# Optimization experiments

Hardware: AMD Instinct MI355X
Metric: run time of the kernel (lower is better)

## Reference

```python
import jax, jax.numpy as jnp
import numpy as np

T = 35        # points per voxel
D, H, W = 10, 400, 352  # voxel grid (KITTI car setting)
EPS = 1e-5    # BatchNorm eps


def setup_inputs() -> dict:
    key = jax.random.key(0)
    ks = jax.random.split(key, 10)
    K = 15000  # non-empty voxels in the frame
    feature = jax.random.normal(ks[0], (K, T, 7), jnp.float32)
    # realistic padding: each voxel has 5..35 valid points, rest zero
    npts = jax.random.randint(ks[1], (K,), 5, T + 1)
    valid = jnp.arange(T)[None, :] < npts[:, None]
    feature = feature * valid[:, :, None].astype(jnp.float32)
    c_b = jnp.zeros((K, 1), jnp.int32)
    c_d = jax.random.randint(ks[2], (K, 1), 0, D).astype(jnp.int32)
    c_h = jax.random.randint(ks[3], (K, 1), 0, H).astype(jnp.int32)
    c_w = jax.random.randint(ks[4], (K, 1), 0, W).astype(jnp.int32)
    coordinate = jnp.concatenate([c_b, c_d, c_h, c_w], axis=1)
    W1 = jax.random.normal(ks[5], (7, 16), jnp.float32) * 0.1
    b1 = jnp.zeros((16,), jnp.float32)
    g1 = jnp.ones((16,), jnp.float32)
    be1 = jnp.zeros((16,), jnp.float32)
    W2 = jax.random.normal(ks[6], (32, 64), jnp.float32) * 0.1
    b2 = jnp.zeros((64,), jnp.float32)
    g2 = jnp.ones((64,), jnp.float32)
    be2 = jnp.zeros((64,), jnp.float32)
    return {"feature": feature, "coordinate": coordinate, "bs": 1,
            "W1": W1, "b1": b1, "g1": g1, "be1": be1,
            "W2": W2, "b2": b2, "g2": g2, "be2": be2}


def _vfe(x, mask, Wm, b, g, be):
    # Linear + ReLU per point: [K, T, cin] -> [K, T, cmid]
    pw = jax.nn.relu(jnp.einsum('ktc,cd->ktd', x, Wm) + b)
    # BatchNorm1d (training mode): per-channel stats over (K, T), biased var
    mu = pw.mean(axis=(0, 1))
    var = pw.var(axis=(0, 1))
    pw = (pw - mu) * jax.lax.rsqrt(var + EPS) * g + be
    # max over points, broadcast-concat (VoxelNet VFE)
    agg = pw.max(axis=1, keepdims=True)               # [K, 1, cmid]
    cat = jnp.concatenate([pw, jnp.broadcast_to(agg, pw.shape)], axis=-1)
    return cat * mask  # mask padded points


def reference(feature, coordinate, bs, W1, b1, g1, be1, W2, b2, g2, be2):
    # mask: point is valid if its channel-wise max != 0 (as in original)
    vmax = feature.max(axis=2, keepdims=True)          # [K, T, 1]
    mask = (vmax != 0).astype(feature.dtype)
    x = _vfe(feature, mask, W1, b1, g1, be1)           # [K, T, 32]
    x = _vfe(x, mask, W2, b2, g2, be2)                 # [K, T, 128]
    voxelwise = x.max(axis=1)                          # [K, 128]
    # scatter into dense grid (sparse COO -> to_dense sums duplicates)
    out = jnp.zeros((bs, D, H, W, 128), feature.dtype)
    out = out.at[coordinate[:, 0], coordinate[:, 1],
                 coordinate[:, 2], coordinate[:, 3]].add(voxelwise)
    return out
```

## Files before the change

### kernel.cpp

```cpp
#include <hip/hip_runtime.h>
#include <math.h>

#define KVOX 15000
#define TP 35
#define CIN 7
#define CM1 16
#define CM2 64
#define NPTS (KVOX * TP)
#define DD 10
#define HH 400
#define WWID 352
#define NCELL (DD * HH * WWID)
#define EPSBN 1e-5f
#define NB1 256
#define NBV 3750
#define NBW 2048

typedef float vfloat4 __attribute__((ext_vector_type(4)));
typedef int   vint4   __attribute__((ext_vector_type(4)));
typedef short bf16x8  __attribute__((ext_vector_type(8)));
typedef float f32x4   __attribute__((ext_vector_type(4)));

__device__ inline unsigned short f2b(float x)
{
    unsigned int u = __float_as_uint(x);
    unsigned int r = (u + 0x7FFFu + ((u >> 16) & 1u)) >> 16;
    return (unsigned short)r;
}

#define NT4 (NCELL / 4)
__global__ __launch_bounds__(256) void init_kernel(vint4* __restrict__ table4)
{
    int i = blockIdx.x * 256 + threadIdx.x;
    table4[i] = (vint4){0x7FFFFFFF, 0x7FFFFFFF, 0x7FFFFFFF, 0x7FFFFFFF};
}

__global__ __launch_bounds__(256) void stats1_kernel(
    const float* __restrict__ feat, const int* __restrict__ coord,
    const float* __restrict__ W1, const float* __restrict__ b1,
    float* __restrict__ partial1, int* __restrict__ table)
{
    __shared__ float w1s[CIN * CM1];
    __shared__ float b1s[CM1];
    __shared__ float red[4][32];
    int tid = threadIdx.x;
    if (tid < CIN * CM1) w1s[tid] = W1[tid];
    if (tid < CM1) b1s[tid] = b1[tid];

    int g = blockIdx.x * 256 + tid;
    if (g < KVOX) {
        int cell = (coord[g * 4 + 1] * HH + coord[g * 4 + 2]) * WWID + coord[g * 4 + 3];
        atomicMin(&table[cell], g);
    }
    __syncthreads();

    float s[CM1], q[CM1];
#pragma unroll
    for (int c = 0; c < CM1; ++c) { s[c] = 0.f; q[c] = 0.f; }

    for (int i = blockIdx.x * 256 + tid; i < NPTS; i += NB1 * 256) {
        float f[CIN];
#pragma unroll
        for (int j = 0; j < CIN; ++j) f[j] = feat[(size_t)i * CIN + j];
#pragma unroll
        for (int c = 0; c < CM1; ++c) {
            float acc = b1s[c];
#pragma unroll
            for (int j = 0; j < CIN; ++j) acc = fmaf(f[j], w1s[j * CM1 + c], acc);
            float pw = fmaxf(acc, 0.f);
            s[c] += pw; q[c] += pw * pw;
        }
    }
#pragma unroll
    for (int c = 0; c < CM1; ++c) {
#pragma unroll
        for (int off = 32; off > 0; off >>= 1) {
            s[c] += __shfl_xor(s[c], off);
            q[c] += __shfl_xor(q[c], off);
        }
    }
    int wid = tid >> 6, lane = tid & 63;
    if (lane == 0) {
#pragma unroll
        for (int c = 0; c < CM1; ++c) { red[wid][c] = s[c]; red[wid][CM1 + c] = q[c]; }
    }
    __syncthreads();
    if (tid < 32)
        partial1[blockIdx.x * 32 + tid] =
            red[0][tid] + red[1][tid] + red[2][tid] + red[3][tid];
}

__global__ __launch_bounds__(256) void reduce1_kernel(
    const float* __restrict__ partial1, const float* __restrict__ g1,
    const float* __restrict__ be1, float* __restrict__ coef1)
{
    __shared__ float acc[8][32];
    __shared__ float tot[32];
    int tid = threadIdx.x;
    int c = tid & 31, part = tid >> 5;
    float v = 0.f;
    for (int b = part; b < NB1; b += 8) v += partial1[b * 32 + c];
    acc[part][c] = v;
    __syncthreads();
    if (tid < 32) {
        float t = 0.f;
#pragma unroll
        for (int p = 0; p < 8; ++p) t += acc[p][tid];
        tot[tid] = t;
    }
    __syncthreads();
    if (tid < CM1) {
        float inv = 1.f / (float)NPTS;
        float mu = tot[tid] * inv;
        float var = tot[CM1 + tid] * inv - mu * mu;
        float a = g1[tid] * rsqrtf(var + EPSBN);
        coef1[tid] = a;
        coef1[CM1 + tid] = be1[tid] - mu * a;
    }
}

__global__ __launch_bounds__(256) void vfe_once_kernel(
    const float* __restrict__ feat,
    const float* __restrict__ W1g, const float* __restrict__ b1g,
    const float* __restrict__ coef1,
    const float* __restrict__ W2g, const float* __restrict__ b2g,
    float* __restrict__ partial2,
    float* __restrict__ ext,
    int*   __restrict__ flags,
    vfloat4* __restrict__ compact4)
{
    __shared__ float sfeat[4][256];
    __shared__ vint4 sct4[4][288];
    __shared__ float smask[4][48];
    __shared__ float red2[4][2 * CM2];

    int tid = threadIdx.x, wid = tid >> 6, lane = tid & 63;
    int k = blockIdx.x * 4 + wid;
    int tg = lane >> 4, c1 = lane & 15;

    float w1r[CIN];
#pragma unroll
    for (int j = 0; j < CIN; ++j) w1r[j] = W1g[j * CM1 + c1];
    float b1r = b1g[c1];
    float a1r = coef1[c1], d1r = coef1[CM1 + c1];

    bf16x8 bfr[4];
    float bias[4];
#pragma unroll
    for (int nt = 0; nt < 4; ++nt) {
        bias[nt] = b2g[nt * 16 + c1];
#pragma unroll
        for (int j = 0; j < 8; ++j)
            bfr[nt][j] = (short)f2b(W2g[(tg * 8 + j) * 64 + nt * 16 + c1]);
    }

    float* F = sfeat[wid];
    unsigned short* CT = (unsigned short*)sct4[wid];
    float* M = smask[wid];

    for (int i = lane; i < TP * CIN; i += 64)
        F[i] = feat[(size_t)k * (TP * CIN) + i];
    {
        vint4 z = {0, 0, 0, 0};
        vint4* pz = (vint4*)(CT + 35 * 48);
        pz[lane] = z;
        if (lane < 14) pz[64 + lane] = z;
        if (lane < 13) M[35 + lane] = 0.f;
    }

    float maxv = -INFINITY;
#pragma unroll
    for (int it = 0; it < 9; ++it) {
        int t = tg + 4 * it;
        if (t < TP) {
            float fv0 = F[t * CIN];
            float m7 = fv0;
            float acc = fmaf(fv0, w1r[0], b1r);
#pragma unroll
            for (int j = 1; j < CIN; ++j) {
                float fv = F[t * CIN + j];
                m7 = fmaxf(m7, fv);
                acc = fmaf(fv, w1r[j], acc);
            }
            float maskv = (m7 != 0.f) ? 1.f : 0.f;
            float pw = fmaxf(acc, 0.f);
            float bn = fmaf(pw, a1r, d1r);
            maxv = fmaxf(maxv, bn);
            CT[t * 48 + c1] = f2b(bn * maskv);
            if (c1 == 0) M[t] = maskv;
        }
    }
    maxv = fmaxf(maxv, __shfl_xor(maxv, 16));
    maxv = fmaxf(maxv, __shfl_xor(maxv, 32));
#pragma unroll
    for (int it = 0; it < 9; ++it) {
        int t = tg + 4 * it;
        if (t < TP) CT[t * 48 + 16 + c1] = f2b(maxv * M[t]);
    }

    f32x4 acc[3][4] = {};
#pragma unroll
    for (int mt = 0; mt < 3; ++mt) {
        bf16x8 a = ((bf16x8*)sct4[wid])[(16 * mt + c1) * 6 + tg];
#pragma unroll
        for (int nt = 0; nt < 4; ++nt)
            acc[mt][nt] = __builtin_amdgcn_mfma_f32_16x16x32_bf16(
                a, bfr[nt], acc[mt][nt], 0, 0, 0);
    }

    float s[4] = {0.f, 0.f, 0.f, 0.f}, q[4] = {0.f, 0.f, 0.f, 0.f};
    float mxv[4], mnv[4], mxa[4], mna[4];
#pragma unroll
    for (int nt = 0; nt < 4; ++nt) {
        mxv[nt] = -INFINITY; mnv[nt] = INFINITY;
        mxa[nt] = -INFINITY; mna[nt] = INFINITY;
    }
    float mmin = 1.f;
#pragma unroll
    for (int mt = 0; mt < 3; ++mt) {
#pragma unroll
        for (int r = 0; r < 4; ++r) {
            int row = 16 * mt + tg * 4 + r;
            bool live = row < TP;
            float mk = M[row];
            if (live) mmin = fminf(mmin, mk);
            bool vld = live && (mk != 0.f);
#pragma unroll
            for (int nt = 0; nt < 4; ++nt) {
                float pw = fmaxf(acc[mt][nt][r] + bias[nt], 0.f);
                if (live) {
                    s[nt] += pw; q[nt] += pw * pw;
                    mxa[nt] = fmaxf(mxa[nt], pw);
                    mna[nt] = fminf(mna[nt], pw);
                }
                if (vld) {
                    mxv[nt] = fmaxf(mxv[nt], pw);
                    mnv[nt] = fminf(mnv[nt], pw);
                }
            }
        }
    }
#pragma unroll
    for (int nt = 0; nt < 4; ++nt) {
        s[nt] += __shfl_xor(s[nt], 16);  s[nt] += __shfl_xor(s[nt], 32);
        q[nt] += __shfl_xor(q[nt], 16);  q[nt] += __shfl_xor(q[nt], 32);
        mxv[nt] = fmaxf(mxv[nt], __shfl_xor(mxv[nt], 16));
        mxv[nt] = fmaxf(mxv[nt], __shfl_xor(mxv[nt], 32));
        mnv[nt] = fminf(mnv[nt], __shfl_xor(mnv[nt], 16));
        mnv[nt] = fminf(mnv[nt], __shfl_xor(mnv[nt], 32));
        mxa[nt] = fmaxf(mxa[nt], __shfl_xor(mxa[nt], 16));
        mxa[nt] = fmaxf(mxa[nt], __shfl_xor(mxa[nt], 32));
        mna[nt] = fminf(mna[nt], __shfl_xor(mna[nt], 16));
        mna[nt] = fminf(mna[nt], __shfl_xor(mna[nt], 32));
    }
    mmin = fminf(mmin, __shfl_xor(mmin, 16));
    mmin = fminf(mmin, __shfl_xor(mmin, 32));

    float o_mxv = tg == 0 ? mxv[0] : tg == 1 ? mxv[1] : tg == 2 ? mxv[2] : mxv[3];
    float o_mnv = tg == 0 ? mnv[0] : tg == 1 ? mnv[1] : tg == 2 ? mnv[2] : mnv[3];
    float o_mxa = tg == 0 ? mxa[0] : tg == 1 ? mxa[1] : tg == 2 ? mxa[2] : mxa[3];
    float o_mna = tg == 0 ? mna[0] : tg == 1 ? mna[1] : tg == 2 ? mna[2] : mna[3];
    float o_s   = tg == 0 ? s[0]   : tg == 1 ? s[1]   : tg == 2 ? s[2]   : s[3];
    float o_q   = tg == 0 ? q[0]   : tg == 1 ? q[1]   : tg == 2 ? q[2]   : q[3];

    float* E = ext + (size_t)k * 256;
    E[lane] = o_mxv; E[64 + lane] = o_mnv;
    E[128 + lane] = o_mxa; E[192 + lane] = o_mna;
    if (lane == 0) flags[k] = (mmin == 0.f) ? 1 : 0;

    red2[wid][lane] = o_s;
    red2[wid][CM2 + lane] = o_q;
    __syncthreads();
    if (tid < 2 * CM2)
        partial2[(size_t)blockIdx.x * (2 * CM2) + tid] =
            red2[0][tid] + red2[1][tid] + red2[2][tid] + red2[3][tid];

    if (tid < 128)
        compact4[(size_t)blockIdx.x * 128 + tid] = (vfloat4){0.f, 0.f, 0.f, 0.f};
}

__global__ __launch_bounds__(256) void reduce2_kernel(
    const float* __restrict__ partial2, const float* __restrict__ g2,
    const float* __restrict__ be2, float* __restrict__ coef2)
{
    __shared__ float sred[4][2];
    int c = blockIdx.x;
    int tid = threadIdx.x;
    float s = 0.f, q = 0.f;
    for (int r = tid; r < NBV; r += 256) {
        s += partial2[(size_t)r * 128 + c];
        q += partial2[(size_t)r * 128 + CM2 + c];
    }
#pragma unroll
    for (int off = 32; off > 0; off >>= 1) {
        s += __shfl_xor(s, off);
        q += __shfl_xor(q, off);
    }
    int wid = tid >> 6;
    if ((tid & 63) == 0) { sred[wid][0] = s; sred[wid][1] = q; }
    __syncthreads();
    if (tid == 0) {
        float S = sred[0][0] + sred[1][0] + sred[2][0] + sred[3][0];
        float Q = sred[0][1] + sred[1][1] + sred[2][1] + sred[3][1];
        float inv = 1.f / (float)NPTS;
        float mu = S * inv;
        float var = Q * inv - mu * mu;
        float a = g2[c] * rsqrtf(var + EPSBN);
        coef2[c] = a;
        coef2[CM2 + c] = be2[c] - mu * a;
    }
}

__global__ __launch_bounds__(256) void finalize_kernel(
    const float* __restrict__ ext, const int* __restrict__ flags,
    const int* __restrict__ coord, const float* __restrict__ coef2,
    const int* __restrict__ table, float* __restrict__ compact)
{
    int tid = threadIdx.x;
    int k = blockIdx.x * 2 + (tid >> 7);
    int sub = tid & 127;
    int c = sub & 63, half = sub >> 6;
    float a = coef2[c], d = coef2[CM2 + c];
    const float* E = ext + (size_t)k * 256 + half * 128;
    float hi = E[c], lo = E[64 + c];
    float val = (a >= 0.f) ? fmaf(a, hi, d) : fmaf(a, lo, d);
    if (flags[k]) val = fmaxf(val, 0.f);
    int cell = (coord[k * 4 + 1] * HH + coord[k * 4 + 2]) * WWID + coord[k * 4 + 3];
    int w = table[cell];
    atomicAdd(&compact[(size_t)w * 128 + sub], val);
}

__global__ __launch_bounds__(256) void write_kernel(
    vfloat4* __restrict__ out, const int* __restrict__ table,
    const vfloat4* __restrict__ compact4)
{
    const int total = NCELL * 32;
    int stride = NBW * 256;
    for (int i = blockIdx.x * 256 + threadIdx.x; i < total; i += stride) {
        int cell = i >> 5;
        int w = table[cell];
        vfloat4 v = {0.f, 0.f, 0.f, 0.f};
        if (w < KVOX) v = compact4[w * 32 + (i & 31)];
        out[i] = v;
    }
}

extern "C" void kernel_launch(void* const* d_in, const int* in_sizes, int n_in,
                              void* d_out, int out_size, void* d_ws, size_t ws_size,
                              hipStream_t stream)
{
    const float* feat = (const float*)d_in[0];
    const int*   coord = (const int*)d_in[1];
    const float* W1  = (const float*)d_in[3];
    const float* b1  = (const float*)d_in[4];
    const float* g1  = (const float*)d_in[5];
    const float* be1 = (const float*)d_in[6];
    const float* W2  = (const float*)d_in[7];
    const float* b2  = (const float*)d_in[8];
    const float* g2  = (const float*)d_in[9];
    const float* be2 = (const float*)d_in[10];
    float* out = (float*)d_out;

    int*   table    = (int*)d_ws;
    float* compact  = (float*)d_ws + NCELL;
    float* ext      = compact + (size_t)KVOX * 128;
    float* partial1 = ext + (size_t)KVOX * 256;
    float* partial2 = partial1 + NB1 * 32;
    int*   flags    = (int*)(partial2 + NBV * 128);
    float* coef1    = (float*)(flags + KVOX);
    float* coef2    = coef1 + 32;

    init_kernel<<<NT4 / 256, 256, 0, stream>>>((vint4*)table);
    stats1_kernel<<<NB1, 256, 0, stream>>>(feat, coord, W1, b1, partial1, table);
    reduce1_kernel<<<1, 256, 0, stream>>>(partial1, g1, be1, coef1);
    vfe_once_kernel<<<NBV, 256, 0, stream>>>(feat, W1, b1, coef1, W2, b2,
                                             partial2, ext, flags,
                                             (vfloat4*)compact);
    reduce2_kernel<<<CM2, 256, 0, stream>>>(partial2, g2, be2, coef2);
    finalize_kernel<<<KVOX / 2, 256, 0, stream>>>(ext, flags, coord, coef2,
                                                  table, compact);
    write_kernel<<<NBW, 256, 0, stream>>>((vfloat4*)out, table, (vfloat4*)compact);
}
```

Before: 789.0 us.

## Zero output directly and scatter-add voxels into it, dropping cell table

Replaces the cell-to-voxel lookup table, compact buffer and table-driven dense write with a plain streaming zero-fill of the output followed by atomic adds of each voxel's features straight into the dense grid. This removes the table initialisation, the atomicMin pass, the compact buffer zeroing and the per-element table reads in the write pass. It relies on the output being zeroed within each call and uses atomics on global output memory.

```diff
diff --git a/kernel.cpp b/kernel.cpp
--- a/kernel.cpp
+++ b/kernel.cpp
@@ -14,7 +14,7 @@
 #define EPSBN 1e-5f
 #define NB1 256
 #define NBV 3750
-#define NBW 2048
+#define NBZ 2048
 
 typedef float vfloat4 __attribute__((ext_vector_type(4)));
 typedef int   vint4   __attribute__((ext_vector_type(4)));
@@ -28,17 +28,18 @@
     return (unsigned short)r;
 }
 
-#define NT4 (NCELL / 4)
-__global__ __launch_bounds__(256) void init_kernel(vint4* __restrict__ table4)
-{
-    int i = blockIdx.x * 256 + threadIdx.x;
-    table4[i] = (vint4){0x7FFFFFFF, 0x7FFFFFFF, 0x7FFFFFFF, 0x7FFFFFFF};
+__global__ __launch_bounds__(256) void zero_kernel(vfloat4* __restrict__ out, int n4)
+{
+    const vfloat4 z = {0.f, 0.f, 0.f, 0.f};
+    int stride = NBZ * 256;
+    for (int i = blockIdx.x * 256 + threadIdx.x; i < n4; i += stride)
+        out[i] = z;
 }
 
 __global__ __launch_bounds__(256) void stats1_kernel(
-    const float* __restrict__ feat, const int* __restrict__ coord,
+    const float* __restrict__ feat,
     const float* __restrict__ W1, const float* __restrict__ b1,
-    float* __restrict__ partial1, int* __restrict__ table)
+    float* __restrict__ partial1)
 {
     __shared__ float w1s[CIN * CM1];
     __shared__ float b1s[CM1];
@@ -46,12 +47,6 @@
     int tid = threadIdx.x;
     if (tid < CIN * CM1) w1s[tid] = W1[tid];
     if (tid < CM1) b1s[tid] = b1[tid];
-
-    int g = blockIdx.x * 256 + tid;
-    if (g < KVOX) {
-        int cell = (coord[g * 4 + 1] * HH + coord[g * 4 + 2]) * WWID + coord[g * 4 + 3];
-        atomicMin(&table[cell], g);
-    }
     __syncthreads();
 
     float s[CM1], q[CM1];
@@ -126,8 +121,7 @@
     const float* __restrict__ W2g, const float* __restrict__ b2g,
     float* __restrict__ partial2,
     float* __restrict__ ext,
-    int*   __restrict__ flags,
-    vfloat4* __restrict__ compact4)
+    int*   __restrict__ flags)
 {
     __shared__ float sfeat[4][256];
     __shared__ vint4 sct4[4][288];
@@ -274,9 +268,6 @@
     if (tid < 2 * CM2)
         partial2[(size_t)blockIdx.x * (2 * CM2) + tid] =
             red2[0][tid] + red2[1][tid] + red2[2][tid] + red2[3][tid];
-
-    if (tid < 128)
-        compact4[(size_t)blockIdx.x * 128 + tid] = (vfloat4){0.f, 0.f, 0.f, 0.f};
 }
 
 __global__ __launch_bounds__(256) void reduce2_kernel(
@@ -314,7 +305,7 @@
 __global__ __launch_bounds__(256) void finalize_kernel(
     const float* __restrict__ ext, const int* __restrict__ flags,
     const int* __restrict__ coord, const float* __restrict__ coef2,
-    const int* __restrict__ table, float* __restrict__ compact)
+    float* __restrict__ out)
 {
     int tid = threadIdx.x;
     int k = blockIdx.x * 2 + (tid >> 7);
@@ -325,24 +316,9 @@
     float hi = E[c], lo = E[64 + c];
     float val = (a >= 0.f) ? fmaf(a, hi, d) : fmaf(a, lo, d);
     if (flags[k]) val = fmaxf(val, 0.f);
-    int cell = (coord[k * 4 + 1] * HH + coord[k * 4 + 2]) * WWID + coord[k * 4 + 3];
-    int w = table[cell];
-    atomicAdd(&compact[(size_t)w * 128 + sub], val);
-}
-
-__global__ __launch_bounds__(256) void write_kernel(
-    vfloat4* __restrict__ out, const int* __restrict__ table,
-    const vfloat4* __restrict__ compact4)
-{
-    const int total = NCELL * 32;
-    int stride = NBW * 256;
-    for (int i = blockIdx.x * 256 + threadIdx.x; i < total; i += stride) {
-        int cell = i >> 5;
-        int w = table[cell];
-        vfloat4 v = {0.f, 0.f, 0.f, 0.f};
-        if (w < KVOX) v = compact4[w * 32 + (i & 31)];
-        out[i] = v;
-    }
+    size_t base = (size_t)((coord[k * 4 + 1] * HH + coord[k * 4 + 2]) * WWID
+                           + coord[k * 4 + 3]) * 128;
+    atomicAdd(&out[base + sub], val);
 }
 
 extern "C" void kernel_launch(void* const* d_in, const int* in_sizes, int n_in,
@@ -361,23 +337,19 @@
     const float* be2 = (const float*)d_in[10];
     float* out = (float*)d_out;
 
-    int*   table    = (int*)d_ws;
-    float* compact  = (float*)d_ws + NCELL;
-    float* ext      = compact + (size_t)KVOX * 128;
+    float* ext      = (float*)d_ws;
     float* partial1 = ext + (size_t)KVOX * 256;
     float* partial2 = partial1 + NB1 * 32;
     int*   flags    = (int*)(partial2 + NBV * 128);
     float* coef1    = (float*)(flags + KVOX);
     float* coef2    = coef1 + 32;
 
-    init_kernel<<<NT4 / 256, 256, 0, stream>>>((vint4*)table);
-    stats1_kernel<<<NB1, 256, 0, stream>>>(feat, coord, W1, b1, partial1, table);
+    zero_kernel<<<NBZ, 256, 0, stream>>>((vfloat4*)out, out_size / 4);
+
+    stats1_kernel<<<NB1, 256, 0, stream>>>(feat, W1, b1, partial1);
     reduce1_kernel<<<1, 256, 0, stream>>>(partial1, g1, be1, coef1);
     vfe_once_kernel<<<NBV, 256, 0, stream>>>(feat, W1, b1, coef1, W2, b2,
-                                             partial2, ext, flags,
-                                             (vfloat4*)compact);
+                                             partial2, ext, flags);
     reduce2_kernel<<<CM2, 256, 0, stream>>>(partial2, g2, be2, coef2);
-    finalize_kernel<<<KVOX / 2, 256, 0, stream>>>(ext, flags, coord, coef2,
-                                                  table, compact);
-    write_kernel<<<NBW, 256, 0, stream>>>((vfloat4*)out, table, (vfloat4*)compact);
-}
+    finalize_kernel<<<KVOX / 2, 256, 0, stream>>>(ext, flags, coord, coef2, out);
+}
```

Result: slower. 829.2 us (+5.1%).

## Fuse finalize into dense write and handle duplicate voxels with a fixup pass

Applied to the files above, without the earlier changes.

The per-voxel BN2 affine and max evaluation now happens inside the dense output write kernel, which reads ext directly for the voxel that owns each cell. The compact buffer, its zeroing and the atomic finalize pass are removed. A small fixup kernel afterwards atomically adds the contributions of duplicate voxels that do not own their cell. It also doubles the stats1 block count. This relies on the table storing one representative voxel per cell and on duplicates being rare, and it puts more ext reads inside the large write loop.

```diff
diff --git a/kernel.cpp b/kernel.cpp
--- a/kernel.cpp
+++ b/kernel.cpp
@@ -12,7 +12,7 @@
 #define WWID 352
 #define NCELL (DD * HH * WWID)
 #define EPSBN 1e-5f
-#define NB1 256
+#define NB1 512
 #define NBV 3750
 #define NBW 2048
 
@@ -126,8 +126,7 @@
     const float* __restrict__ W2g, const float* __restrict__ b2g,
     float* __restrict__ partial2,
     float* __restrict__ ext,
-    int*   __restrict__ flags,
-    vfloat4* __restrict__ compact4)
+    int*   __restrict__ flags)
 {
     __shared__ float sfeat[4][256];
     __shared__ vint4 sct4[4][288];
@@ -274,9 +273,6 @@
     if (tid < 2 * CM2)
         partial2[(size_t)blockIdx.x * (2 * CM2) + tid] =
             red2[0][tid] + red2[1][tid] + red2[2][tid] + red2[3][tid];
-
-    if (tid < 128)
-        compact4[(size_t)blockIdx.x * 128 + tid] = (vfloat4){0.f, 0.f, 0.f, 0.f};
 }
 
 __global__ __launch_bounds__(256) void reduce2_kernel(
@@ -311,38 +307,59 @@
     }
 }
 
-__global__ __launch_bounds__(256) void finalize_kernel(
+__global__ __launch_bounds__(256) void write_kernel(
+    vfloat4* __restrict__ out, const int* __restrict__ table,
+    const float* __restrict__ ext, const int* __restrict__ flags,
+    const float* __restrict__ coef2)
+{
+    __shared__ float sa[CM2], sd[CM2];
+    int tid = threadIdx.x;
+    if (tid < CM2) { sa[tid] = coef2[tid]; sd[tid] = coef2[CM2 + tid]; }
+    __syncthreads();
+
+    const int total = NCELL * 32;
+    int stride = NBW * 256;
+    for (int i = blockIdx.x * 256 + tid; i < total; i += stride) {
+        int cell = i >> 5;
+        int w = table[cell];
+        vfloat4 v = {0.f, 0.f, 0.f, 0.f};
+        if (w < KVOX) {
+            int s = i & 31;
+            int half = s >> 4;
+            int c0 = (s & 15) * 4;
+            const float* E = ext + (size_t)w * 256 + half * 128;
+            int fl = flags[w];
+#pragma unroll
+            for (int j = 0; j < 4; ++j) {
+                int c = c0 + j;
+                float a = sa[c], d = sd[c];
+                float hi = E[c], lo = E[64 + c];
+                float val = (a >= 0.f) ? fmaf(a, hi, d) : fmaf(a, lo, d);
+                if (fl) val = fmaxf(val, 0.f);
+                v[j] = val;
+            }
+        }
+        out[i] = v;
+    }
+}
+
+__global__ __launch_bounds__(256) void fixup_kernel(
     const float* __restrict__ ext, const int* __restrict__ flags,
     const int* __restrict__ coord, const float* __restrict__ coef2,
-    const int* __restrict__ table, float* __restrict__ compact)
+    const int* __restrict__ table, float* __restrict__ out)
 {
     int tid = threadIdx.x;
     int k = blockIdx.x * 2 + (tid >> 7);
     int sub = tid & 127;
+    int cell = (coord[k * 4 + 1] * HH + coord[k * 4 + 2]) * WWID + coord[k * 4 + 3];
+    if (table[cell] == k) return;
     int c = sub & 63, half = sub >> 6;
     float a = coef2[c], d = coef2[CM2 + c];
     const float* E = ext + (size_t)k * 256 + half * 128;
     float hi = E[c], lo = E[64 + c];
     float val = (a >= 0.f) ? fmaf(a, hi, d) : fmaf(a, lo, d);
     if (flags[k]) val = fmaxf(val, 0.f);
-    int cell = (coord[k * 4 + 1] * HH + coord[k * 4 + 2]) * WWID + coord[k * 4 + 3];
-    int w = table[cell];
-    atomicAdd(&compact[(size_t)w * 128 + sub], val);
-}
-
-__global__ __launch_bounds__(256) void write_kernel(
-    vfloat4* __restrict__ out, const int* __restrict__ table,
-    const vfloat4* __restrict__ compact4)
-{
-    const int total = NCELL * 32;
-    int stride = NBW * 256;
-    for (int i = blockIdx.x * 256 + threadIdx.x; i < total; i += stride) {
-        int cell = i >> 5;
-        int w = table[cell];
-        vfloat4 v = {0.f, 0.f, 0.f, 0.f};
-        if (w < KVOX) v = compact4[w * 32 + (i & 31)];
-        out[i] = v;
-    }
+    atomicAdd(&out[(size_t)cell * 128 + sub], val);
 }
 
 extern "C" void kernel_launch(void* const* d_in, const int* in_sizes, int n_in,
@@ -362,8 +379,7 @@
     float* out = (float*)d_out;
 
     int*   table    = (int*)d_ws;
-    float* compact  = (float*)d_ws + NCELL;
-    float* ext      = compact + (size_t)KVOX * 128;
+    float* ext      = (float*)d_ws + NCELL;
     float* partial1 = ext + (size_t)KVOX * 256;
     float* partial2 = partial1 + NB1 * 32;
     int*   flags    = (int*)(partial2 + NBV * 128);
@@ -374,10 +390,8 @@
     stats1_kernel<<<NB1, 256, 0, stream>>>(feat, coord, W1, b1, partial1, table);
     reduce1_kernel<<<1, 256, 0, stream>>>(partial1, g1, be1, coef1);
     vfe_once_kernel<<<NBV, 256, 0, stream>>>(feat, W1, b1, coef1, W2, b2,
-                                             partial2, ext, flags,
-                                             (vfloat4*)compact);
+                                             partial2, ext, flags);
     reduce2_kernel<<<CM2, 256, 0, stream>>>(partial2, g2, be2, coef2);
-    finalize_kernel<<<KVOX / 2, 256, 0, stream>>>(ext, flags, coord, coef2,
-                                                  table, compact);
-    write_kernel<<<NBW, 256, 0, stream>>>((vfloat4*)out, table, (vfloat4*)compact);
-}
+    write_kernel<<<NBW, 256, 0, stream>>>((vfloat4*)out, table, ext, flags, coef2);
+    fixup_kernel<<<KVOX / 2, 256, 0, stream>>>(ext, flags, coord, coef2, table, out);
+}
```

New measurement: 817.4 us. 1.04x slower.
